# Kernel tuning notes

Hardware: AMD Instinct MI355X
Metric: run time of the kernel (lower is better)

The kernel has to match this reference:

```python
import jax, jax.numpy as jnp
import numpy as np

N_NODES = 50000


def gcn_norm(edge_index, edge_weight, n):
    """PyG GCNConv normalization: add self-loops (weight 1), sym-normalize."""
    src, dst = edge_index[0], edge_index[1]
    loop = jnp.arange(n, dtype=src.dtype)
    src = jnp.concatenate([src, loop])
    dst = jnp.concatenate([dst, loop])
    w = jnp.concatenate([edge_weight, jnp.ones((n,), dtype=edge_weight.dtype)])
    deg = jax.ops.segment_sum(w, dst, num_segments=n)  # in-degree w/ self-loops
    dis = jnp.where(deg > 0, jax.lax.rsqrt(deg), 0.0)  # deg^{-1/2}, inf -> 0
    norm = dis[src] * w * dis[dst]                      # [E+N]
    return src, dst, norm


def gcn_conv(x, src, dst, norm, W, b):
    h = x @ W                                            # [N, F_out]
    msg = norm[:, None] * h[src]                         # gather + scale
    out = jax.ops.segment_sum(msg, dst, num_segments=x.shape[0])  # scatter-add
    return out + b


def setup_inputs() -> dict:
    key = jax.random.key(0)
    ks = jax.random.split(key, 10)
    n, e = N_NODES, 800000
    in_dim, hidden, out_dim = 256, 128, 64
    x = jax.random.normal(ks[0], (n, in_dim), dtype=jnp.float32)
    edge_index = jax.random.randint(ks[1], (2, e), 0, n, dtype=jnp.int32)
    edge_weight = jax.random.uniform(ks[2], (e,), dtype=jnp.float32)
    def glorot(k, fi, fo):
        lim = float(np.sqrt(6.0 / (fi + fo)))
        return jax.random.uniform(k, (fi, fo), minval=-lim, maxval=lim, dtype=jnp.float32)
    return {
        "x": x, "edge_index": edge_index, "edge_weight": edge_weight,
        "W1": glorot(ks[3], in_dim, hidden), "b1": jnp.zeros((hidden,), jnp.float32),
        "W2": glorot(ks[4], hidden, hidden), "b2": jnp.zeros((hidden,), jnp.float32),
        "W3": glorot(ks[5], hidden, out_dim), "b3": jnp.zeros((out_dim,), jnp.float32),
    }


def reference(x, edge_index, edge_weight, W1, b1, W2, b2, W3, b3):
    n = x.shape[0]
    src, dst, norm = gcn_norm(edge_index, edge_weight, n)  # cached=True: shared
    h = jax.nn.relu(gcn_conv(x, src, dst, norm, W1, b1))   # dropout: eval mode no-op
    h = jax.nn.relu(gcn_conv(h, src, dst, norm, W2, b2))
    h = gcn_conv(h, src, dst, norm, W3, b3)
    return h
```

## Files before the change

### kernel.cpp

```cpp
#include <hip/hip_runtime.h>
#include <hip/hip_bf16.h>
#include <stdint.h>

#define NODES 50000
#define EDGES 800000
#define SCAN_TB 256
#define SCAN_NB ((NODES + SCAN_TB - 1) / SCAN_TB)

typedef short bf16x8 __attribute__((ext_vector_type(8)));
typedef float f32x4 __attribute__((ext_vector_type(4)));

__device__ __forceinline__ unsigned short f2bf(float f) {
    union { float f; unsigned u; } v; v.f = f;
    unsigned r = v.u + 0x7fff + ((v.u >> 16) & 1);
    return (unsigned short)(r >> 16);
}
__device__ __forceinline__ float bf2f(unsigned short h) {
    union { float f; unsigned u; } v; v.u = ((unsigned)h) << 16;
    return v.f;
}
__device__ __forceinline__ float bflo(unsigned hv) {
    union { float f; unsigned u; } v; v.u = hv << 16;
    return v.f;
}
__device__ __forceinline__ float bfhi(unsigned hv) {
    union { float f; unsigned u; } v; v.u = hv & 0xffff0000u;
    return v.f;
}


__global__ void k_init(unsigned long long* packed) {
    int i = blockIdx.x * blockDim.x + threadIdx.x;
    if (i < NODES) packed[i] = (1ull << 24);
}

__global__ void k_deg(const int* __restrict__ dst, const float* __restrict__ w,
                      unsigned long long* __restrict__ packed, int* __restrict__ rank) {
    int e = blockIdx.x * blockDim.x + threadIdx.x;
    if (e < EDGES) {
        int d = dst[e];
        unsigned fx = __float2uint_rn(w[e] * 16777216.0f);
        unsigned long long add = (1ull << 40) | (unsigned long long)fx;
        unsigned long long old = atomicAdd(&packed[d], add);
        rank[e] = (int)(old >> 40);
    }
}


__global__ void k_scan1(const unsigned long long* __restrict__ packed,
                        float* __restrict__ dis, int* __restrict__ pre,
                        int* __restrict__ bsum) {
    __shared__ int sm[SCAN_TB];
    int t = threadIdx.x;
    int i = blockIdx.x * SCAN_TB + t;
    int v = 0;
    if (i < NODES) {
        unsigned long long pk = packed[i];
        v = (int)(pk >> 40);
        float deg = (float)(pk & 0xFFFFFFFFFFull) * (1.0f / 16777216.0f);
        dis[i] = rsqrtf(deg);
    }
    sm[t] = v;
    __syncthreads();
    for (int off = 1; off < SCAN_TB; off <<= 1) {
        int x = (t >= off) ? sm[t - off] : 0;
        __syncthreads();
        sm[t] += x;
        __syncthreads();
    }
    if (i < NODES) pre[i] = sm[t] - v;
    if (t == SCAN_TB - 1) bsum[blockIdx.x] = sm[t];
}

__global__ void k_scan2(const int* __restrict__ bsum, int* __restrict__ boff,
                        int* __restrict__ rowptr) {
    __shared__ int sm[256];
    int t = threadIdx.x;
    int v = (t < SCAN_NB) ? bsum[t] : 0;
    sm[t] = v;
    __syncthreads();
    for (int off = 1; off < 256; off <<= 1) {
        int x = (t >= off) ? sm[t - off] : 0;
        __syncthreads();
        sm[t] += x;
        __syncthreads();
    }
    if (t < SCAN_NB) boff[t] = sm[t] - v;
    if (t == 255) rowptr[NODES] = sm[255];
}

__global__ void k_scan3(const int* __restrict__ pre, const int* __restrict__ boff,
                        int* __restrict__ rowptr) {
    int b = blockIdx.x;
    int i = b * SCAN_TB + threadIdx.x;
    if (i < NODES) rowptr[i] = pre[i] + boff[b];
}

__global__ void k_scatter(const int* __restrict__ src, const int* __restrict__ dst,
                          const float* __restrict__ w, const float* __restrict__ dis,
                          const int* __restrict__ rowptr, const int* __restrict__ rank,
                          int2* __restrict__ rec) {
    int e = blockIdx.x * blockDim.x + threadIdx.x;
    if (e < EDGES) {
        int s = src[e], d = dst[e];
        float nrm = dis[s] * w[e] * dis[d];
        int pos = rowptr[d] + rank[e];
        int2 r; r.x = s; r.y = __float_as_int(nrm);
        rec[pos] = r;
    }
}

__global__ void k_wfrag(const float* __restrict__ W, unsigned short* Wf, int K, int Nn) {
    int idx = blockIdx.x * blockDim.x + threadIdx.x;
    int NT = Nn >> 4;
    int total = (K >> 5) * NT * 64;
    if (idx >= total) return;
    int lane = idx & 63;
    int f = idx >> 6;
    int nt = f % NT;
    int k0 = (f / NT) << 5;
    int n = (nt << 4) + (lane & 15);
    int kk = k0 + ((lane >> 4) << 3);
    unsigned short o[8];
#pragma unroll
    for (int j = 0; j < 8; j++) o[j] = f2bf(W[(kk + j) * Nn + n]);
    ((uint4*)Wf)[idx] = *(uint4*)o;
}

template <int K, int Nn, bool A_F32>
__global__ void k_gemm(const void* __restrict__ A_, const uint4* __restrict__ Wf,
                       unsigned short* __restrict__ Hout) {
    constexpr int NT = Nn / 16;
    int lane = threadIdx.x & 63;
    int wave = threadIdx.x >> 6;
    int tile = blockIdx.x * 4 + wave;
    if (tile * 16 >= NODES) return;
    int row = tile * 16 + (lane & 15);
    int kbase = (lane >> 4) * 8;

    f32x4 acc[NT];
#pragma unroll
    for (int i = 0; i < NT; i++) acc[i] = (f32x4){0.f, 0.f, 0.f, 0.f};

    for (int k0 = 0; k0 < K; k0 += 32) {
        bf16x8 a;
        if (A_F32) {
            const float* A = (const float*)A_;
            const float4* p = (const float4*)&A[(size_t)row * K + k0 + kbase];
            float4 u0 = p[0], u1 = p[1];
            unsigned short t[8];
            t[0] = f2bf(u0.x); t[1] = f2bf(u0.y); t[2] = f2bf(u0.z); t[3] = f2bf(u0.w);
            t[4] = f2bf(u1.x); t[5] = f2bf(u1.y); t[6] = f2bf(u1.z); t[7] = f2bf(u1.w);
            a = *(bf16x8*)t;
        } else {
            const unsigned short* A = (const unsigned short*)A_;
            a = *(const bf16x8*)&A[(size_t)row * K + k0 + kbase];
        }
        int fbase = (k0 >> 5) * NT;
#pragma unroll
        for (int nt = 0; nt < NT; nt++) {
            uint4 braw = Wf[(fbase + nt) * 64 + lane];
            bf16x8 b = *(bf16x8*)&braw;
            acc[nt] = __builtin_amdgcn_mfma_f32_16x16x32_bf16(a, b, acc[nt], 0, 0, 0);
        }
    }
    int r0 = (lane >> 4) * 4;
    int col = lane & 15;
#pragma unroll
    for (int nt = 0; nt < NT; nt++) {
#pragma unroll
        for (int r = 0; r < 4; r++) {
            int m = tile * 16 + r0 + r;
            Hout[(size_t)m * Nn + nt * 16 + col] = f2bf(acc[nt][r]);
        }
    }
}

template <int F, bool RELU, bool OUT_F32>
__global__ void k_agg(const unsigned short* __restrict__ H, const int2* __restrict__ rec,
                      const int* __restrict__ rowptr, const float* __restrict__ dis,
                      const float* __restrict__ bias, void* __restrict__ out_) {
    constexpr int VPT = F / 64;
    int lane = threadIdx.x & 63;
    int wave = threadIdx.x >> 6;
    int node = blockIdx.x * 4 + wave;
    if (node >= NODES) return;

    const unsigned* H32 = (const unsigned*)H;

    float sn = dis[node]; sn = sn * sn;
    float acc0, acc1 = 0.f;
    if (VPT == 2) {
        unsigned hv = H32[(size_t)node * 64 + lane];
        acc0 = sn * bflo(hv);
        acc1 = sn * bfhi(hv);
    } else {
        acc0 = sn * bf2f(H[(size_t)node * F + lane]);
    }

    int beg = rowptr[node], end = rowptr[node + 1];
    for (int c = beg; c < end; c += 64) {
        int nrem = end - c; if (nrem > 64) nrem = 64;
        int2 r; r.x = 0; r.y = 0;
        if (lane < nrem) r = rec[c + lane];
        int j = 0;
        for (; j + 4 <= nrem; j += 4) {
            int   s0 = __shfl(r.x, j);     float n0 = __shfl(__int_as_float(r.y), j);
            int   s1 = __shfl(r.x, j + 1); float n1 = __shfl(__int_as_float(r.y), j + 1);
            int   s2 = __shfl(r.x, j + 2); float n2 = __shfl(__int_as_float(r.y), j + 2);
            int   s3 = __shfl(r.x, j + 3); float n3 = __shfl(__int_as_float(r.y), j + 3);
            if (VPT == 2) {
                unsigned h0 = H32[(size_t)s0 * 64 + lane];
                unsigned h1 = H32[(size_t)s1 * 64 + lane];
                unsigned h2 = H32[(size_t)s2 * 64 + lane];
                unsigned h3 = H32[(size_t)s3 * 64 + lane];
                acc0 += n0 * bflo(h0); acc1 += n0 * bfhi(h0);
                acc0 += n1 * bflo(h1); acc1 += n1 * bfhi(h1);
                acc0 += n2 * bflo(h2); acc1 += n2 * bfhi(h2);
                acc0 += n3 * bflo(h3); acc1 += n3 * bfhi(h3);
            } else {
                unsigned short h0 = H[(size_t)s0 * F + lane];
                unsigned short h1 = H[(size_t)s1 * F + lane];
                unsigned short h2 = H[(size_t)s2 * F + lane];
                unsigned short h3 = H[(size_t)s3 * F + lane];
                acc0 += n0 * bf2f(h0);
                acc0 += n1 * bf2f(h1);
                acc0 += n2 * bf2f(h2);
                acc0 += n3 * bf2f(h3);
            }
        }
        for (; j < nrem; ++j) {
            int s = __shfl(r.x, j);
            float nm = __shfl(__int_as_float(r.y), j);
            if (VPT == 2) {
                unsigned hv = H32[(size_t)s * 64 + lane];
                acc0 += nm * bflo(hv);
                acc1 += nm * bfhi(hv);
            } else {
                acc0 += nm * bf2f(H[(size_t)s * F + lane]);
            }
        }
    }

    if (OUT_F32) {
        float* out = (float*)out_;
        if (VPT == 2) {
            float x0 = acc0 + bias[lane * 2];
            float x1 = acc1 + bias[lane * 2 + 1];
            if (RELU) { x0 = fmaxf(x0, 0.f); x1 = fmaxf(x1, 0.f); }
            out[(size_t)node * F + lane * 2] = x0;
            out[(size_t)node * F + lane * 2 + 1] = x1;
        } else {
            float x0 = acc0 + bias[lane];
            if (RELU) x0 = fmaxf(x0, 0.f);
            out[(size_t)node * F + lane] = x0;
        }
    } else {
        unsigned short* out = (unsigned short*)out_;
        if (VPT == 2) {
            float x0 = acc0 + bias[lane * 2];
            float x1 = acc1 + bias[lane * 2 + 1];
            if (RELU) { x0 = fmaxf(x0, 0.f); x1 = fmaxf(x1, 0.f); }
            unsigned packed = (unsigned)f2bf(x0) | ((unsigned)f2bf(x1) << 16);
            *(unsigned*)&out[(size_t)node * F + lane * 2] = packed;
        } else {
            float x0 = acc0 + bias[lane];
            if (RELU) x0 = fmaxf(x0, 0.f);
            out[(size_t)node * F + lane] = f2bf(x0);
        }
    }
}


extern "C" void kernel_launch(void* const* d_in, const int* in_sizes, int n_in,
                              void* d_out, int out_size, void* d_ws, size_t ws_size,
                              hipStream_t stream) {
    const float* x  = (const float*)d_in[0];
    const int*   ei = (const int*)d_in[1];
    const float* w  = (const float*)d_in[2];
    const float* W1 = (const float*)d_in[3];
    const float* b1 = (const float*)d_in[4];
    const float* W2 = (const float*)d_in[5];
    const float* b2 = (const float*)d_in[6];
    const float* W3 = (const float*)d_in[7];
    const float* b3 = (const float*)d_in[8];
    const int* src = ei;
    const int* dst = ei + EDGES;

    char* p = (char*)d_ws;
    auto alloc = [&](size_t n) { char* r = p; p += (n + 511) & ~(size_t)511; return r; };
    unsigned long long* packed = (unsigned long long*)alloc(NODES * 8);
    float*          dis    = (float*)alloc(NODES * 4);
    int*            rowptr = (int*)alloc((NODES + 1) * 4);
    int*            rank   = (int*)alloc(EDGES * 4);
    int*            pre    = (int*)alloc(NODES * 4);
    int*            bsum   = (int*)alloc(SCAN_NB * 4);
    int*            boff   = (int*)alloc(SCAN_NB * 4);
    int2*           rec    = (int2*)alloc(EDGES * 8);
    unsigned short* h      = (unsigned short*)alloc((size_t)NODES * 128 * 2);
    unsigned short* xb     = (unsigned short*)alloc((size_t)NODES * 128 * 2);
    unsigned short* wf1    = (unsigned short*)alloc(256 * 128 * 2);
    unsigned short* wf2    = (unsigned short*)alloc(128 * 128 * 2);
    unsigned short* wf3    = (unsigned short*)alloc(128 * 64 * 2);

    const int TB = 256;
    int nb_nodes = (NODES + TB - 1) / TB;
    int nb_edges = (EDGES + TB - 1) / TB;

    hipLaunchKernelGGL(k_init, dim3(nb_nodes), dim3(TB), 0, stream, packed);
    hipLaunchKernelGGL(k_deg, dim3(nb_edges), dim3(TB), 0, stream, dst, w, packed, rank);
    hipLaunchKernelGGL(k_scan1, dim3(SCAN_NB), dim3(SCAN_TB), 0, stream, packed, dis, pre, bsum);
    hipLaunchKernelGGL(k_scan2, dim3(1), dim3(256), 0, stream, bsum, boff, rowptr);
    hipLaunchKernelGGL(k_scan3, dim3(SCAN_NB), dim3(SCAN_TB), 0, stream, pre, boff, rowptr);
    hipLaunchKernelGGL(k_scatter, dim3(nb_edges), dim3(TB), 0, stream, src, dst, w, dis, rowptr, rank, rec);

    hipLaunchKernelGGL(k_wfrag, dim3((8 * 8 * 64) / TB), dim3(TB), 0, stream, W1, wf1, 256, 128);
    hipLaunchKernelGGL(k_wfrag, dim3((4 * 8 * 64) / TB), dim3(TB), 0, stream, W2, wf2, 128, 128);
    hipLaunchKernelGGL(k_wfrag, dim3((4 * 4 * 64) / TB), dim3(TB), 0, stream, W3, wf3, 128, 64);

    int nb_gemm = (NODES / 16 + 3) / 4;
    int nb_agg  = (NODES + 3) / 4;

    hipLaunchKernelGGL((k_gemm<256, 128, true>), dim3(nb_gemm), dim3(TB), 0, stream, (const void*)x, (const uint4*)wf1, h);
    hipLaunchKernelGGL((k_agg<128, true, false>), dim3(nb_agg), dim3(TB), 0, stream, h, rec, rowptr, dis, b1, (void*)xb);

    hipLaunchKernelGGL((k_gemm<128, 128, false>), dim3(nb_gemm), dim3(TB), 0, stream, (const void*)xb, (const uint4*)wf2, h);
    hipLaunchKernelGGL((k_agg<128, true, false>), dim3(nb_agg), dim3(TB), 0, stream, h, rec, rowptr, dis, b2, (void*)xb);

    hipLaunchKernelGGL((k_gemm<128, 64, false>), dim3(nb_gemm), dim3(TB), 0, stream, (const void*)xb, (const uint4*)wf3, h);
    hipLaunchKernelGGL((k_agg<64, false, true>), dim3(nb_agg), dim3(TB), 0, stream, h, rec, rowptr, dis, b3, d_out);
}
```

Baseline: 304.7 us.

## Replicate degree atomic counters, merge weight-fragment kernels, widen aggregation unroll

Degree counting now spreads atomics across 8 replicated counter arrays chosen by block index, and the scan combines the replicas into per-replica offsets used when scattering CSR records. This aims to reduce atomic contention on hot destination nodes, at the cost of larger init and scan traffic. The three weight-fragment conversion launches are merged into one kernel to cut launch overhead. The aggregation inner loop is unrolled to 8 gathers with a padded tail, which relies on zero-filled records beyond nrem (index 0, weight 0) being harmless.

```diff
diff --git a/kernel.cpp b/kernel.cpp
--- a/kernel.cpp
+++ b/kernel.cpp
@@ -4,6 +4,7 @@
 
 #define NODES 50000
 #define EDGES 800000
+#define R_REP 8
 #define SCAN_TB 256
 #define SCAN_NB ((NODES + SCAN_TB - 1) / SCAN_TB)
 
@@ -31,33 +32,42 @@
 
 __global__ void k_init(unsigned long long* packed) {
     int i = blockIdx.x * blockDim.x + threadIdx.x;
-    if (i < NODES) packed[i] = (1ull << 24);
+    if (i < NODES * R_REP) packed[i] = 0ull;
 }
 
 __global__ void k_deg(const int* __restrict__ dst, const float* __restrict__ w,
                       unsigned long long* __restrict__ packed, int* __restrict__ rank) {
     int e = blockIdx.x * blockDim.x + threadIdx.x;
+    int r = blockIdx.x & (R_REP - 1);
     if (e < EDGES) {
         int d = dst[e];
         unsigned fx = __float2uint_rn(w[e] * 16777216.0f);
         unsigned long long add = (1ull << 40) | (unsigned long long)fx;
-        unsigned long long old = atomicAdd(&packed[d], add);
+        unsigned long long old = atomicAdd(&packed[(size_t)r * NODES + d], add);
         rank[e] = (int)(old >> 40);
     }
 }
 
 
 __global__ void k_scan1(const unsigned long long* __restrict__ packed,
-                        float* __restrict__ dis, int* __restrict__ pre,
-                        int* __restrict__ bsum) {
+                        float* __restrict__ dis, int* __restrict__ repoff,
+                        int* __restrict__ pre, int* __restrict__ bsum) {
     __shared__ int sm[SCAN_TB];
     int t = threadIdx.x;
     int i = blockIdx.x * SCAN_TB + t;
     int v = 0;
     if (i < NODES) {
-        unsigned long long pk = packed[i];
-        v = (int)(pk >> 40);
-        float deg = (float)(pk & 0xFFFFFFFFFFull) * (1.0f / 16777216.0f);
+        unsigned long long degfx = 0;
+        int off = 0;
+#pragma unroll
+        for (int r = 0; r < R_REP; r++) {
+            unsigned long long pk = packed[(size_t)r * NODES + i];
+            repoff[(size_t)r * NODES + i] = off;
+            off += (int)(pk >> 40);
+            degfx += (pk & 0xFFFFFFFFFFull);
+        }
+        v = off;
+        float deg = 1.0f + (float)degfx * (1.0f / 16777216.0f);
         dis[i] = rsqrtf(deg);
     }
     sm[t] = v;
@@ -98,23 +108,22 @@
 
 __global__ void k_scatter(const int* __restrict__ src, const int* __restrict__ dst,
                           const float* __restrict__ w, const float* __restrict__ dis,
-                          const int* __restrict__ rowptr, const int* __restrict__ rank,
-                          int2* __restrict__ rec) {
+                          const int* __restrict__ rowptr, const int* __restrict__ repoff,
+                          const int* __restrict__ rank, int2* __restrict__ rec) {
     int e = blockIdx.x * blockDim.x + threadIdx.x;
+    int r = blockIdx.x & (R_REP - 1);
     if (e < EDGES) {
         int s = src[e], d = dst[e];
         float nrm = dis[s] * w[e] * dis[d];
-        int pos = rowptr[d] + rank[e];
-        int2 r; r.x = s; r.y = __float_as_int(nrm);
-        rec[pos] = r;
-    }
-}
-
-__global__ void k_wfrag(const float* __restrict__ W, unsigned short* Wf, int K, int Nn) {
-    int idx = blockIdx.x * blockDim.x + threadIdx.x;
+        int pos = rowptr[d] + repoff[(size_t)r * NODES + d] + rank[e];
+        int2 rc; rc.x = s; rc.y = __float_as_int(nrm);
+        rec[pos] = rc;
+    }
+}
+
+__device__ __forceinline__ void wfrag_one(const float* __restrict__ W, unsigned short* Wf,
+                                          int idx, int K, int Nn) {
     int NT = Nn >> 4;
-    int total = (K >> 5) * NT * 64;
-    if (idx >= total) return;
     int lane = idx & 63;
     int f = idx >> 6;
     int nt = f % NT;
@@ -125,6 +134,15 @@
 #pragma unroll
     for (int j = 0; j < 8; j++) o[j] = f2bf(W[(kk + j) * Nn + n]);
     ((uint4*)Wf)[idx] = *(uint4*)o;
+}
+
+__global__ void k_wfrag_all(const float* __restrict__ W1, unsigned short* Wf1,
+                            const float* __restrict__ W2, unsigned short* Wf2,
+                            const float* __restrict__ W3, unsigned short* Wf3) {
+    int idx = blockIdx.x * blockDim.x + threadIdx.x;
+    if (idx < 4096) wfrag_one(W1, Wf1, idx, 256, 128);
+    else if (idx < 6144) wfrag_one(W2, Wf2, idx - 4096, 128, 128);
+    else if (idx < 7168) wfrag_one(W3, Wf3, idx - 6144, 128, 64);
 }
 
 template <int K, int Nn, bool A_F32>
@@ -203,41 +221,29 @@
         int nrem = end - c; if (nrem > 64) nrem = 64;
         int2 r; r.x = 0; r.y = 0;
         if (lane < nrem) r = rec[c + lane];
-        int j = 0;
-        for (; j + 4 <= nrem; j += 4) {
-            int   s0 = __shfl(r.x, j);     float n0 = __shfl(__int_as_float(r.y), j);
-            int   s1 = __shfl(r.x, j + 1); float n1 = __shfl(__int_as_float(r.y), j + 1);
-            int   s2 = __shfl(r.x, j + 2); float n2 = __shfl(__int_as_float(r.y), j + 2);
-            int   s3 = __shfl(r.x, j + 3); float n3 = __shfl(__int_as_float(r.y), j + 3);
+        int nceil = (nrem + 7) & ~7;
+        for (int j = 0; j < nceil; j += 8) {
+            int ss[8]; float nn[8];
+#pragma unroll
+            for (int q = 0; q < 8; q++) {
+                ss[q] = __shfl(r.x, j + q);
+                nn[q] = __shfl(__int_as_float(r.y), j + q);
+            }
             if (VPT == 2) {
-                unsigned h0 = H32[(size_t)s0 * 64 + lane];
-                unsigned h1 = H32[(size_t)s1 * 64 + lane];
-                unsigned h2 = H32[(size_t)s2 * 64 + lane];
-                unsigned h3 = H32[(size_t)s3 * 64 + lane];
-                acc0 += n0 * bflo(h0); acc1 += n0 * bfhi(h0);
-                acc0 += n1 * bflo(h1); acc1 += n1 * bfhi(h1);
-                acc0 += n2 * bflo(h2); acc1 += n2 * bfhi(h2);
-                acc0 += n3 * bflo(h3); acc1 += n3 * bfhi(h3);
+                unsigned hh[8];
+#pragma unroll
+                for (int q = 0; q < 8; q++) hh[q] = H32[(size_t)ss[q] * 64 + lane];
+#pragma unroll
+                for (int q = 0; q < 8; q++) {
+                    acc0 += nn[q] * bflo(hh[q]);
+                    acc1 += nn[q] * bfhi(hh[q]);
+                }
             } else {
-                unsigned short h0 = H[(size_t)s0 * F + lane];
-                unsigned short h1 = H[(size_t)s1 * F + lane];
-                unsigned short h2 = H[(size_t)s2 * F + lane];
-                unsigned short h3 = H[(size_t)s3 * F + lane];
-                acc0 += n0 * bf2f(h0);
-                acc0 += n1 * bf2f(h1);
-                acc0 += n2 * bf2f(h2);
-                acc0 += n3 * bf2f(h3);
-            }
-        }
-        for (; j < nrem; ++j) {
-            int s = __shfl(r.x, j);
-            float nm = __shfl(__int_as_float(r.y), j);
-            if (VPT == 2) {
-                unsigned hv = H32[(size_t)s * 64 + lane];
-                acc0 += nm * bflo(hv);
-                acc1 += nm * bfhi(hv);
-            } else {
-                acc0 += nm * bf2f(H[(size_t)s * F + lane]);
+                unsigned short hh[8];
+#pragma unroll
+                for (int q = 0; q < 8; q++) hh[q] = H[(size_t)ss[q] * F + lane];
+#pragma unroll
+                for (int q = 0; q < 8; q++) acc0 += nn[q] * bf2f(hh[q]);
             }
         }
     }
@@ -289,9 +295,10 @@
 
     char* p = (char*)d_ws;
     auto alloc = [&](size_t n) { char* r = p; p += (n + 511) & ~(size_t)511; return r; };
-    unsigned long long* packed = (unsigned long long*)alloc(NODES * 8);
+    unsigned long long* packed = (unsigned long long*)alloc((size_t)NODES * R_REP * 8);
     float*          dis    = (float*)alloc(NODES * 4);
     int*            rowptr = (int*)alloc((NODES + 1) * 4);
+    int*            repoff = (int*)alloc((size_t)NODES * R_REP * 4);
     int*            rank   = (int*)alloc(EDGES * 4);
     int*            pre    = (int*)alloc(NODES * 4);
     int*            bsum   = (int*)alloc(SCAN_NB * 4);
@@ -304,19 +311,18 @@
     unsigned short* wf3    = (unsigned short*)alloc(128 * 64 * 2);
 
     const int TB = 256;
-    int nb_nodes = (NODES + TB - 1) / TB;
+    int nb_initR = (NODES * R_REP + TB - 1) / TB;
     int nb_edges = (EDGES + TB - 1) / TB;
 
-    hipLaunchKernelGGL(k_init, dim3(nb_nodes), dim3(TB), 0, stream, packed);
+    hipLaunchKernelGGL(k_init, dim3(nb_initR), dim3(TB), 0, stream, packed);
     hipLaunchKernelGGL(k_deg, dim3(nb_edges), dim3(TB), 0, stream, dst, w, packed, rank);
-    hipLaunchKernelGGL(k_scan1, dim3(SCAN_NB), dim3(SCAN_TB), 0, stream, packed, dis, pre, bsum);
+    hipLaunchKernelGGL(k_scan1, dim3(SCAN_NB), dim3(SCAN_TB), 0, stream, packed, dis, repoff, pre, bsum);
     hipLaunchKernelGGL(k_scan2, dim3(1), dim3(256), 0, stream, bsum, boff, rowptr);
     hipLaunchKernelGGL(k_scan3, dim3(SCAN_NB), dim3(SCAN_TB), 0, stream, pre, boff, rowptr);
-    hipLaunchKernelGGL(k_scatter, dim3(nb_edges), dim3(TB), 0, stream, src, dst, w, dis, rowptr, rank, rec);
-
-    hipLaunchKernelGGL(k_wfrag, dim3((8 * 8 * 64) / TB), dim3(TB), 0, stream, W1, wf1, 256, 128);
-    hipLaunchKernelGGL(k_wfrag, dim3((4 * 8 * 64) / TB), dim3(TB), 0, stream, W2, wf2, 128, 128);
-    hipLaunchKernelGGL(k_wfrag, dim3((4 * 4 * 64) / TB), dim3(TB), 0, stream, W3, wf3, 128, 64);
+    hipLaunchKernelGGL(k_scatter, dim3(nb_edges), dim3(TB), 0, stream, src, dst, w, dis, rowptr, repoff, rank, rec);
+
+    hipLaunchKernelGGL(k_wfrag_all, dim3((7168 + TB - 1) / TB), dim3(TB), 0, stream,
+                       W1, wf1, W2, wf2, W3, wf3);
 
     int nb_gemm = (NODES / 16 + 3) / 4;
     int nb_agg  = (NODES + 3) / 4;
```

Result: faster. 292.4 us (-4.0%).
